# Optimization experiments

Hardware: AMD Instinct MI355X
Metric: run time of the kernel (lower is better)

Reference implementation:

```python
import jax, jax.numpy as jnp
import numpy as np

N, E = 100000, 3200000
IN_DIM, PRED_DIM, REL_NUM = 128, 16, 50
H, L = 4, 3          # heads per layer, num_layers
NEG_SLOPE = 0.2      # SALayer attention leaky_relu slope


def setup_inputs() -> dict:
    key = jax.random.key(0)
    ks = jax.random.split(key, 9)
    hid = IN_DIM // 2
    return {
        "inputs": jax.random.normal(ks[0], (N, IN_DIM), jnp.float32),
        "centrality": jax.random.uniform(ks[1], (N,), jnp.float32),
        # per-head scoring MLP: Linear(in,in/2) -> ReLU -> Linear(in/2,1)
        "W1": jax.random.normal(ks[2], (H, hid, IN_DIM), jnp.float32) * 0.05,
        "b1": jnp.zeros((H, hid), jnp.float32),
        "W2": jax.random.normal(ks[3], (H, hid), jnp.float32) * 0.05,
        "b2": jnp.zeros((H,), jnp.float32),
        "rel_emb": jax.random.normal(ks[4], (REL_NUM, PRED_DIM), jnp.float32),
        # per-layer predicate->attention projection (pred_dim -> heads)
        "W_pred": jax.random.normal(ks[5], (L, PRED_DIM, H), jnp.float32) * 0.1,
        "gamma": jnp.ones((1, H), jnp.float32),
        "beta": jnp.zeros((1, H), jnp.float32),
        "edge_types": jax.random.randint(ks[6], (E,), 0, REL_NUM),
        "src": jax.random.randint(ks[7], (E,), 0, N),
        "dst": jax.random.randint(ks[8], (E,), 0, N),
    }


def _edge_softmax(e, dst, n):
    # numerically stable softmax over incoming edges of each dst node, per head
    m = jax.ops.segment_max(e, dst, num_segments=n)          # (N,H)
    ex = jnp.exp(e - m[dst])                                  # (E,H)
    s = jax.ops.segment_sum(ex, dst, num_segments=n)          # (N,H)
    return ex / s[dst]


def reference(inputs, centrality, W1, b1, W2, b2, rel_emb, W_pred,
              gamma, beta, edge_types, src, dst):
    n = inputs.shape[0]
    # multi-head scoring MLPs -> per-node per-head scalar scores (N,H)
    hid = jax.nn.relu(jnp.einsum('ni,khi->nkh', inputs, W1) + b1)  # (N,H,hid)
    h = jnp.einsum('nkh,kh->nk', hid, W2) + b2                     # (N,H)
    ef = rel_emb[edge_types]                                       # (E,P)
    for l in range(L):
        # SALayer: predicate-based attention, edge softmax, aggregate src scores
        e = jax.nn.leaky_relu(ef @ W_pred[l], NEG_SLOPE)           # (E,H)
        a = _edge_softmax(e, dst, n)                               # (E,H)
        h = jax.nn.relu(jax.ops.segment_sum(a * h[src], dst, num_segments=n))
        if l != L - 1:
            # flatten(1).mean(-1,keepdim).repeat(1,H)
            h = jnp.repeat(jnp.mean(h, axis=-1, keepdims=True), H, axis=-1)
    logits = h  # (N,H)
    # centrality scaling: leaky_relu(((c*gamma+beta)*logits).mean(-1,keepdim))
    scaled = (centrality[:, None] * gamma + beta) * logits
    return jax.nn.leaky_relu(jnp.mean(scaled, axis=-1, keepdims=True), 0.01)
```

## Files before the change

### kernel.cpp

```cpp
#include <hip/hip_runtime.h>
#include <cstdint>
#include <cstddef>

#define NHEAD 4
#define HID 64
#define NCOL 256
#define INDIM 128
#define PREDDIM 16
#define RELNUM 50
#define NLAYER 3
#define ECHUNK 8192
#define DSHIFT 9
#define DPB 512
#define MAXBUCK 256
#define MAXCHUNK 512
#define SPLIT_BLOCKS 32
#define MLP_GRID 512

typedef _Float16 half8 __attribute__((ext_vector_type(8)));
typedef float float4v __attribute__((ext_vector_type(4)));
typedef const __attribute__((address_space(1))) void gvoid_t;
typedef __attribute__((address_space(3))) void lvoid_t;

__global__ __launch_bounds__(256, 2) void mlp_mfma_kernel(
    const float* __restrict__ X, const _Float16* __restrict__ Wh,
    const _Float16* __restrict__ Wl, const float* __restrict__ b1,
    const float* __restrict__ W2, const float* __restrict__ b2,
    float* __restrict__ h0, int N)
{
    __shared__ float Xs[2][64][128];

    const int tid  = threadIdx.x;
    const int w    = tid >> 6;
    const int lane = tid & 63;
    const int n16  = lane & 15;
    const int q    = lane >> 4;
    const int swzm = (n16 & 7) << 4;

    half8 bh[4][4], bl[4][4];
    float b1v[4], w2v[4];
    #pragma unroll
    for (int ct = 0; ct < 4; ct++) {
        const int c = w * 64 + ct * 16 + n16;
        const _Float16* pb = Wh + (size_t)c * INDIM + q * 8;
        const _Float16* pl = Wl + (size_t)c * INDIM + q * 8;
        #pragma unroll
        for (int ks = 0; ks < 4; ks++) {
            bh[ct][ks] = *reinterpret_cast<const half8*>(pb + ks * 32);
            bl[ct][ks] = *reinterpret_cast<const half8*>(pl + ks * 32);
        }
        b1v[ct] = b1[c];
        w2v[ct] = W2[c];
    }
    #pragma unroll
    for (int ct = 0; ct < 4; ct++) {
        #pragma unroll
        for (int ks = 0; ks < 4; ks++)
            asm volatile("" : "+v"(bh[ct][ks]), "+v"(bl[ct][ks]));
        asm volatile("" : "+v"(b1v[ct]), "+v"(w2v[ct]));
    }

    const float bk = b2[w];
    const int ntiles = (N + 63) >> 6;

    auto stage = [&](int tile, int buf) {
        #pragma unroll
        for (int i = 0; i < 8; i++) {
            const int lds_off = i * 4096 + w * 1024 + lane * 16;
            const int node = lds_off >> 9;
            const int scol = (lds_off & 511) ^ ((node & 7) << 4);
            const int gn = min(tile * 64 + node, N - 1);
            const char* gsrc = (const char*)X + (size_t)gn * 512 + scol;
            char* ldst = (char*)(&Xs[buf][0][0]) + lds_off;
            __builtin_amdgcn_global_load_lds((gvoid_t*)gsrc, (lvoid_t*)ldst,
                                             16, 0, 0);
        }
    };

    int tile = blockIdx.x;
    if (tile >= ntiles) return;
    int buf = 0;
    stage(tile, 0);
    asm volatile("s_waitcnt vmcnt(0)" ::: "memory");
    __syncthreads();

    while (true) {
        const int nxt = tile + MLP_GRID;
        if (nxt < ntiles) stage(nxt, buf ^ 1);

        #pragma unroll 1
        for (int mt = 0; mt < 4; mt++) {
            const char* rowp = (const char*)(&Xs[buf][mt * 16 + n16][0]);
            half8 ah[4], al[4];
            #pragma unroll
            for (int ks = 0; ks < 4; ks++) {
                const int cb0 = ks * 128 + q * 32;
                float4v r0 = *reinterpret_cast<const float4v*>(rowp + (cb0 ^ swzm));
                float4v r1 = *reinterpret_cast<const float4v*>(rowp + ((cb0 + 16) ^ swzm));
                #pragma unroll
                for (int j = 0; j < 4; j++) {
                    float x = r0[j];
                    _Float16 hh = (_Float16)x;
                    ah[ks][j] = hh;
                    al[ks][j] = (_Float16)((x - (float)hh) * 2048.0f);
                    x = r1[j];
                    hh = (_Float16)x;
                    ah[ks][4 + j] = hh;
                    al[ks][4 + j] = (_Float16)((x - (float)hh) * 2048.0f);
                }
            }

            float s[4] = {0.f, 0.f, 0.f, 0.f};
            #pragma unroll
            for (int ct = 0; ct < 4; ct++) {
                float4v acc = (float4v){0.f,0.f,0.f,0.f};
                float4v aca = (float4v){0.f,0.f,0.f,0.f};
                float4v acb = (float4v){0.f,0.f,0.f,0.f};
                #pragma unroll
                for (int ks = 0; ks < 4; ks++) {
                    acc = __builtin_amdgcn_mfma_f32_16x16x32_f16(ah[ks], bh[ct][ks], acc, 0, 0, 0);
                    aca = __builtin_amdgcn_mfma_f32_16x16x32_f16(ah[ks], bl[ct][ks], aca, 0, 0, 0);
                    acb = __builtin_amdgcn_mfma_f32_16x16x32_f16(al[ks], bh[ct][ks], acb, 0, 0, 0);
                }
                #pragma unroll
                for (int r = 0; r < 4; r++) {
                    float v = acc[r] + (aca[r] + acb[r]) * (1.0f / 2048.0f) + b1v[ct];
                    s[r] += fmaxf(v, 0.f) * w2v[ct];
                }
            }

            #pragma unroll
            for (int r = 0; r < 4; r++) {
                float v = s[r];
                v += __shfl_down(v, 8, 16);
                v += __shfl_down(v, 4, 16);
                v += __shfl_down(v, 2, 16);
                v += __shfl_down(v, 1, 16);
                if (n16 == 0) {
                    int node = tile * 64 + mt * 16 + q * 4 + r;
                    if (node < N) h0[(size_t)node * NHEAD + w] = v + bk;
                }
            }
        }

        if (nxt >= ntiles) break;
        asm volatile("s_waitcnt vmcnt(0)" ::: "memory");
        __syncthreads();
        tile = nxt;
        buf ^= 1;
    }
}

__global__ __launch_bounds__(1024) void bucket_count_fused_kernel(
    const int* __restrict__ dst, int* __restrict__ blockhist, int E,
    int nbuck, int nb,
    const float* __restrict__ rel_emb, const float* __restrict__ W_pred,
    float* __restrict__ wtab,
    const float* __restrict__ W1, _Float16* __restrict__ Wh,
    _Float16* __restrict__ Wl)
{
    __shared__ int hist[MAXBUCK];
    const int tid = threadIdx.x;
    const int bx  = blockIdx.x;

    if (bx < nb) {
        if (tid < MAXBUCK) hist[tid] = 0;
        __syncthreads();
        const int base = bx * ECHUNK;
        const int end  = min(base + ECHUNK, E);
        const int nvec = (end - base) >> 2;
        const int4* d4p = reinterpret_cast<const int4*>(dst + base);
        for (int g = tid; g < nvec; g += 1024) {
            int4 d = d4p[g];
            atomicAdd(&hist[d.x >> DSHIFT], 1);
            atomicAdd(&hist[d.y >> DSHIFT], 1);
            atomicAdd(&hist[d.z >> DSHIFT], 1);
            atomicAdd(&hist[d.w >> DSHIFT], 1);
        }
        for (int i = base + (nvec << 2) + tid; i < end; i += 1024)
            atomicAdd(&hist[dst[i] >> DSHIFT], 1);
        __syncthreads();
        if (tid < nbuck) blockhist[(size_t)tid * nb + bx] = hist[tid];
    } else if (bx == nb) {
        const int idx = tid;
        if (idx < NLAYER * RELNUM * NHEAD) {
            int h = idx & 3;
            int qq = idx >> 2;
            int t = qq % RELNUM;
            int l = qq / RELNUM;
            float acc = 0.f;
            #pragma unroll
            for (int p = 0; p < PREDDIM; p++)
                acc = fmaf(rel_emb[t * PREDDIM + p],
                           W_pred[l * PREDDIM * NHEAD + p * NHEAD + h], acc);
            float e = (acc >= 0.f) ? acc : 0.2f * acc;
            wtab[idx] = __expf(e);
        }
    } else {
        const int i = (bx - nb - 1) * 1024 + tid;
        float v = W1[i];
        _Float16 h = (_Float16)v;
        Wh[i] = h;
        Wl[i] = (_Float16)((v - (float)h) * 2048.0f);
    }
}

__global__ __launch_bounds__(512) void scan_chunks_kernel(
    const int* __restrict__ blockhist, int* __restrict__ blockbase,
    int* __restrict__ bucket_size, int nb)
{
    __shared__ int s[MAXCHUNK];
    const int b = blockIdx.x;
    const int t = threadIdx.x;
    int v = (t < nb) ? blockhist[(size_t)b * nb + t] : 0;
    s[t] = v;
    __syncthreads();
    for (int off = 1; off < MAXCHUNK; off <<= 1) {
        int u = (t >= off) ? s[t - off] : 0;
        __syncthreads();
        s[t] += u;
        __syncthreads();
    }
    if (t < nb) blockbase[(size_t)b * nb + t] = s[t] - v;
    if (t == MAXCHUNK - 1) bucket_size[b] = s[t];
}

__global__ __launch_bounds__(256) void scan_buckets_kernel(
    const int* __restrict__ bucket_size, int* __restrict__ bucket_start, int nbuck)
{
    __shared__ int s[256];
    const int t = threadIdx.x;
    int v = (t < nbuck) ? bucket_size[t] : 0;
    s[t] = v;
    __syncthreads();
    for (int off = 1; off < 256; off <<= 1) {
        int u = (t >= off) ? s[t - off] : 0;
        __syncthreads();
        s[t] += u;
        __syncthreads();
    }
    if (t < nbuck) bucket_start[t] = s[t] - v;
}

__global__ __launch_bounds__(1024) void bucket_scatter_kernel(
    const int* __restrict__ src, const int* __restrict__ dst,
    const int* __restrict__ types, const int* __restrict__ blockbase,
    const int* __restrict__ bucket_start, int* __restrict__ bucketed,
    int E, int nbuck, int nb)
{
    __shared__ int lbase[MAXBUCK];
    __shared__ int cur[MAXBUCK];
    const int tid = threadIdx.x;
    if (tid < MAXBUCK) {
        lbase[tid] = (tid < nbuck)
            ? blockbase[(size_t)tid * nb + blockIdx.x] + bucket_start[tid] : 0;
        cur[tid] = 0;
    }
    __syncthreads();
    const int base = blockIdx.x * ECHUNK;
    const int end  = min(base + ECHUNK, E);
    const int nvec = (end - base) >> 2;
    const int4* s4p = reinterpret_cast<const int4*>(src + base);
    const int4* d4p = reinterpret_cast<const int4*>(dst + base);
    const int4* t4p = reinterpret_cast<const int4*>(types + base);
    for (int g = tid; g < nvec; g += 1024) {
        int4 sv = s4p[g], dv = d4p[g], tv = t4p[g];
        int b, r;
        b = dv.x >> DSHIFT; r = atomicAdd(&cur[b], 1);
        bucketed[lbase[b] + r] = sv.x | (tv.x << 17) | ((dv.x & (DPB - 1)) << 23);
        b = dv.y >> DSHIFT; r = atomicAdd(&cur[b], 1);
        bucketed[lbase[b] + r] = sv.y | (tv.y << 17) | ((dv.y & (DPB - 1)) << 23);
        b = dv.z >> DSHIFT; r = atomicAdd(&cur[b], 1);
        bucketed[lbase[b] + r] = sv.z | (tv.z << 17) | ((dv.z & (DPB - 1)) << 23);
        b = dv.w >> DSHIFT; r = atomicAdd(&cur[b], 1);
        bucketed[lbase[b] + r] = sv.w | (tv.w << 17) | ((dv.w & (DPB - 1)) << 23);
    }
    for (int i = base + (nvec << 2) + tid; i < end; i += 1024) {
        int d = dst[i];
        int b = d >> DSHIFT;
        int r = atomicAdd(&cur[b], 1);
        bucketed[lbase[b] + r] = src[i] | (types[i] << 17) | ((d & (DPB - 1)) << 23);
    }
}

__global__ __launch_bounds__(1024) void bucket_to_csr_kernel(
    const int* __restrict__ bucket_start, const int* __restrict__ bucket_size,
    const int* __restrict__ bucketed, int* __restrict__ sorted,
    int* __restrict__ row_start, int* __restrict__ deg, int N)
{
    __shared__ int cnt[DPB];
    __shared__ int sc[DPB];
    __shared__ int rs[DPB];
    __shared__ int cur[DPB];
    const int tid = threadIdx.x;
    const int b   = blockIdx.x;
    const int d0  = b << DSHIFT;
    const int nd  = min(DPB, N - d0);
    const int s0  = bucket_start[b];
    const int ne  = bucket_size[b];

    if (tid < DPB) { cnt[tid] = 0; cur[tid] = 0; }
    __syncthreads();
    for (int i = tid; i < ne; i += 1024)
        atomicAdd(&cnt[((unsigned)bucketed[s0 + i] >> 23) & (DPB - 1)], 1);
    __syncthreads();
    int v = 0;
    if (tid < DPB) { v = cnt[tid]; sc[tid] = v; }
    __syncthreads();
    for (int off = 1; off < DPB; off <<= 1) {
        int u = (tid < DPB && tid >= off) ? sc[tid - off] : 0;
        __syncthreads();
        if (tid < DPB) sc[tid] += u;
        __syncthreads();
    }
    if (tid < DPB) {
        int ex = sc[tid] - v;
        rs[tid] = s0 + ex;
        if (tid < nd) {
            row_start[d0 + tid] = s0 + ex;
            deg[d0 + tid] = v;
        }
    }
    __syncthreads();
    for (int i = tid; i < ne; i += 1024) {
        int pk = bucketed[s0 + i];
        int d  = ((unsigned)pk >> 23) & (DPB - 1);
        int r  = atomicAdd(&cur[d], 1);
        sorted[rs[d] + r] = pk & 0x7FFFFF;
    }
}

template <int MODE>
__global__ __launch_bounds__(256) void agg_kernel(
    const int* __restrict__ row_start, const int* __restrict__ deg,
    const int* __restrict__ sorted, const float* __restrict__ wt_l,
    const float* __restrict__ hin, float* __restrict__ hout,
    const float* __restrict__ centrality, const float* __restrict__ gamma,
    const float* __restrict__ beta, int N)
{
    __shared__ float4 wt4[RELNUM];
    for (int i = threadIdx.x; i < RELNUM; i += blockDim.x)
        wt4[i] = reinterpret_cast<const float4*>(wt_l)[i];
    __syncthreads();

    int gid = blockIdx.x * blockDim.x + threadIdx.x;
    int d = gid >> 2, j = gid & 3;
    if (d >= N) return;

    int b = row_start[d], n = deg[d];
    float n0 = 0.f, n1 = 0.f, n2 = 0.f, n3 = 0.f;
    float d0 = 0.f, d1 = 0.f, d2 = 0.f, d3 = 0.f;
    for (int i = j; i < n; i += 4) {
        int pk = sorted[b + i];
        int s = pk & 0x1FFFF;
        int t = pk >> 17;
        float4 w4 = wt4[t];
        if (MODE == 0) {
            float4 h4 = *reinterpret_cast<const float4*>(hin + (size_t)s * NHEAD);
            n0 = fmaf(w4.x, h4.x, n0); n1 = fmaf(w4.y, h4.y, n1);
            n2 = fmaf(w4.z, h4.z, n2); n3 = fmaf(w4.w, h4.w, n3);
        } else {
            float hv = hin[s];
            n0 = fmaf(w4.x, hv, n0); n1 = fmaf(w4.y, hv, n1);
            n2 = fmaf(w4.z, hv, n2); n3 = fmaf(w4.w, hv, n3);
        }
        d0 += w4.x; d1 += w4.y; d2 += w4.z; d3 += w4.w;
    }

    #pragma unroll
    for (int k = 1; k <= 2; k <<= 1) {
        n0 += __shfl_xor(n0, k); n1 += __shfl_xor(n1, k);
        n2 += __shfl_xor(n2, k); n3 += __shfl_xor(n3, k);
        d0 += __shfl_xor(d0, k); d1 += __shfl_xor(d1, k);
        d2 += __shfl_xor(d2, k); d3 += __shfl_xor(d3, k);
    }

    if (j == 0) {
        float r0 = (n > 0) ? fmaxf(n0 / d0, 0.f) : 0.f;
        float r1 = (n > 0) ? fmaxf(n1 / d1, 0.f) : 0.f;
        float r2 = (n > 0) ? fmaxf(n2 / d2, 0.f) : 0.f;
        float r3 = (n > 0) ? fmaxf(n3 / d3, 0.f) : 0.f;
        if (MODE == 2) {
            float c = centrality[d];
            r0 *= (c * gamma[0] + beta[0]);
            r1 *= (c * gamma[1] + beta[1]);
            r2 *= (c * gamma[2] + beta[2]);
            r3 *= (c * gamma[3] + beta[3]);
        }
        float m = (r0 + r1 + r2 + r3) * 0.25f;
        if (MODE < 2) hout[d] = m;
        else          hout[d] = (m > 0.f) ? m : 0.01f * m;
    }
}

extern "C" void kernel_launch(void* const* d_in, const int* in_sizes, int n_in,
                              void* d_out, int out_size, void* d_ws, size_t ws_size,
                              hipStream_t stream)
{
    const float* X          = (const float*)d_in[0];
    const float* centrality = (const float*)d_in[1];
    const float* W1         = (const float*)d_in[2];
    const float* b1         = (const float*)d_in[3];
    const float* W2         = (const float*)d_in[4];
    const float* b2         = (const float*)d_in[5];
    const float* rel_emb    = (const float*)d_in[6];
    const float* W_pred     = (const float*)d_in[7];
    const float* gamma      = (const float*)d_in[8];
    const float* beta       = (const float*)d_in[9];
    const int*   edge_types = (const int*)d_in[10];
    const int*   src        = (const int*)d_in[11];
    const int*   dst        = (const int*)d_in[12];
    float* out = (float*)d_out;

    const int N = in_sizes[1];
    const int E = in_sizes[10];
    const int nbuck = (N + DPB - 1) / DPB;
    const int eb = (E + ECHUNK - 1) / ECHUNK;

    char* ws = (char*)d_ws;
    size_t off = 0;
    auto alloc = [&](size_t bytes) -> void* {
        void* p = ws + off;
        off = (off + bytes + 255) & ~(size_t)255;
        return p;
    };
    int*   deg       = (int*)alloc((size_t)N * 4);
    int*   row_start = (int*)alloc((size_t)N * 4);
    int*   bsize     = (int*)alloc((size_t)MAXBUCK * 4);
    int*   bstart    = (int*)alloc((size_t)MAXBUCK * 4);
    int*   blockhist = (int*)alloc((size_t)nbuck * eb * 4);
    int*   blockbase = (int*)alloc((size_t)nbuck * eb * 4);
    int*   bucketed  = (int*)alloc((size_t)E * 4);
    int*   sorted    = (int*)alloc((size_t)E * 4);
    float* wtab      = (float*)alloc((size_t)NLAYER * RELNUM * NHEAD * 4);
    float* h0        = (float*)alloc((size_t)N * NHEAD * 4);
    float* hs        = (float*)alloc((size_t)N * 4);
    float* hs2       = (float*)alloc((size_t)N * 4);
    _Float16* Wh     = (_Float16*)alloc((size_t)NCOL * INDIM * 2);
    _Float16* Wl     = (_Float16*)alloc((size_t)NCOL * INDIM * 2);
    (void)ws_size; (void)n_in; (void)out_size;

    bucket_count_fused_kernel<<<eb + 1 + SPLIT_BLOCKS, 1024, 0, stream>>>(
        dst, blockhist, E, nbuck, eb, rel_emb, W_pred, wtab, W1, Wh, Wl);
    scan_chunks_kernel<<<nbuck, MAXCHUNK, 0, stream>>>(blockhist, blockbase, bsize, eb);
    scan_buckets_kernel<<<1, 256, 0, stream>>>(bsize, bstart, nbuck);
    bucket_scatter_kernel<<<eb, 1024, 0, stream>>>(src, dst, edge_types, blockbase,
                                                   bstart, bucketed, E, nbuck, eb);
    bucket_to_csr_kernel<<<nbuck, 1024, 0, stream>>>(bstart, bsize, bucketed, sorted,
                                                     row_start, deg, N);

    mlp_mfma_kernel<<<MLP_GRID, 256, 0, stream>>>(X, Wh, Wl, b1, W2, b2, h0, N);

    const int ab = (N * NHEAD + 255) / 256;
    agg_kernel<0><<<ab, 256, 0, stream>>>(row_start, deg, sorted, wtab + 0 * RELNUM * NHEAD,
                                          h0, hs, nullptr, nullptr, nullptr, N);
    agg_kernel<1><<<ab, 256, 0, stream>>>(row_start, deg, sorted, wtab + 1 * RELNUM * NHEAD,
                                          hs, hs2, nullptr, nullptr, nullptr, N);
    agg_kernel<2><<<ab, 256, 0, stream>>>(row_start, deg, sorted, wtab + 2 * RELNUM * NHEAD,
                                          hs2, out, centrality, gamma, beta, N);
}
```

Before: 273.1 us.

## Convert MLP inputs to split-fp16 once at staging into MFMA-ready LDS layout

Replaces async global-to-LDS fp32 staging with register prefetch of the next tile. Each thread converts its slice to hi/lo fp16 once and writes it to LDS in an MFMA operand layout. Previously every wave redid the fp32-to-fp16 split on each read. Now the MFMA loop reads half8 operands directly with an XOR swizzle. The cost is 32 more registers per thread for the prefetch, which may pressure occupancy at 2 blocks/SM, and the load-to-LDS overlap now depends on register prefetch.

Result: slower. 283.3 us (+3.7%).

```diff
diff --git a/kernel.cpp b/kernel.cpp
--- a/kernel.cpp
+++ b/kernel.cpp
@@ -19,8 +19,6 @@
 
 typedef _Float16 half8 __attribute__((ext_vector_type(8)));
 typedef float float4v __attribute__((ext_vector_type(4)));
-typedef const __attribute__((address_space(1))) void gvoid_t;
-typedef __attribute__((address_space(3))) void lvoid_t;
 
 __global__ __launch_bounds__(256, 2) void mlp_mfma_kernel(
     const float* __restrict__ X, const _Float16* __restrict__ Wh,
@@ -28,14 +26,14 @@
     const float* __restrict__ W2, const float* __restrict__ b2,
     float* __restrict__ h0, int N)
 {
-    __shared__ float Xs[2][64][128];
+    __shared__ _Float16 hA[2][4][4][64][8];
+    __shared__ _Float16 lA[2][4][4][64][8];
 
     const int tid  = threadIdx.x;
     const int w    = tid >> 6;
     const int lane = tid & 63;
     const int n16  = lane & 15;
     const int q    = lane >> 4;
-    const int swzm = (n16 & 7) << 4;
 
     half8 bh[4][4], bl[4][4];
     float b1v[4], w2v[4];
@@ -63,51 +61,56 @@
     const float bk = b2[w];
     const int ntiles = (N + 63) >> 6;
 
-    auto stage = [&](int tile, int buf) {
-        #pragma unroll
-        for (int i = 0; i < 8; i++) {
-            const int lds_off = i * 4096 + w * 1024 + lane * 16;
-            const int node = lds_off >> 9;
-            const int scol = (lds_off & 511) ^ ((node & 7) << 4);
-            const int gn = min(tile * 64 + node, N - 1);
-            const char* gsrc = (const char*)X + (size_t)gn * 512 + scol;
-            char* ldst = (char*)(&Xs[buf][0][0]) + lds_off;
-            __builtin_amdgcn_global_load_lds((gvoid_t*)gsrc, (lvoid_t*)ldst,
-                                             16, 0, 0);
-        }
-    };
+    const int mg  = tid >> 2, sks = tid & 3;
+    const int smt = mg >> 4,  sm  = mg & 15;
 
     int tile = blockIdx.x;
     if (tile >= ntiles) return;
+
+    {
+        const int gn = min(tile * 64 + mg, N - 1);
+        const float4* Xp = reinterpret_cast<const float4*>(X + (size_t)gn * INDIM + sks * 32);
+        float4 xr[8];
+        #pragma unroll
+        for (int i = 0; i < 8; i++) xr[i] = Xp[i];
+        #pragma unroll
+        for (int qq = 0; qq < 4; qq++) {
+            float xs[8] = { xr[qq*2].x, xr[qq*2].y, xr[qq*2].z, xr[qq*2].w,
+                            xr[qq*2+1].x, xr[qq*2+1].y, xr[qq*2+1].z, xr[qq*2+1].w };
+            half8 hv, lv;
+            #pragma unroll
+            for (int j = 0; j < 8; j++) {
+                _Float16 hh = (_Float16)xs[j];
+                hv[j] = hh;
+                lv[j] = (_Float16)((xs[j] - (float)hh) * 2048.0f);
+            }
+            const int slot = (qq * 16 + sm) ^ (2 * sks);
+            *reinterpret_cast<half8*>(&hA[0][smt][sks][slot][0]) = hv;
+            *reinterpret_cast<half8*>(&lA[0][smt][sks][slot][0]) = lv;
+        }
+    }
+    __syncthreads();
     int buf = 0;
-    stage(tile, 0);
-    asm volatile("s_waitcnt vmcnt(0)" ::: "memory");
-    __syncthreads();
 
     while (true) {
         const int nxt = tile + MLP_GRID;
-        if (nxt < ntiles) stage(nxt, buf ^ 1);
+
+        float4 xn[8];
+        if (nxt < ntiles) {
+            const int gn = min(nxt * 64 + mg, N - 1);
+            const float4* Xp = reinterpret_cast<const float4*>(X + (size_t)gn * INDIM + sks * 32);
+            #pragma unroll
+            for (int i = 0; i < 8; i++) xn[i] = Xp[i];
+        }
 
         #pragma unroll 1
         for (int mt = 0; mt < 4; mt++) {
-            const char* rowp = (const char*)(&Xs[buf][mt * 16 + n16][0]);
             half8 ah[4], al[4];
             #pragma unroll
-            for (int ks = 0; ks < 4; ks++) {
-                const int cb0 = ks * 128 + q * 32;
-                float4v r0 = *reinterpret_cast<const float4v*>(rowp + (cb0 ^ swzm));
-                float4v r1 = *reinterpret_cast<const float4v*>(rowp + ((cb0 + 16) ^ swzm));
-                #pragma unroll
-                for (int j = 0; j < 4; j++) {
-                    float x = r0[j];
-                    _Float16 hh = (_Float16)x;
-                    ah[ks][j] = hh;
-                    al[ks][j] = (_Float16)((x - (float)hh) * 2048.0f);
-                    x = r1[j];
-                    hh = (_Float16)x;
-                    ah[ks][4 + j] = hh;
-                    al[ks][4 + j] = (_Float16)((x - (float)hh) * 2048.0f);
-                }
+            for (int kk = 0; kk < 4; kk++) {
+                const int slot = lane ^ (2 * kk);
+                ah[kk] = *reinterpret_cast<const half8*>(&hA[buf][mt][kk][slot][0]);
+                al[kk] = *reinterpret_cast<const half8*>(&lA[buf][mt][kk][slot][0]);
             }
 
             float s[4] = {0.f, 0.f, 0.f, 0.f};
@@ -117,10 +120,10 @@
                 float4v aca = (float4v){0.f,0.f,0.f,0.f};
                 float4v acb = (float4v){0.f,0.f,0.f,0.f};
                 #pragma unroll
-                for (int ks = 0; ks < 4; ks++) {
-                    acc = __builtin_amdgcn_mfma_f32_16x16x32_f16(ah[ks], bh[ct][ks], acc, 0, 0, 0);
-                    aca = __builtin_amdgcn_mfma_f32_16x16x32_f16(ah[ks], bl[ct][ks], aca, 0, 0, 0);
-                    acb = __builtin_amdgcn_mfma_f32_16x16x32_f16(al[ks], bh[ct][ks], acb, 0, 0, 0);
+                for (int kk = 0; kk < 4; kk++) {
+                    acc = __builtin_amdgcn_mfma_f32_16x16x32_f16(ah[kk], bh[ct][kk], acc, 0, 0, 0);
+                    aca = __builtin_amdgcn_mfma_f32_16x16x32_f16(ah[kk], bl[ct][kk], aca, 0, 0, 0);
+                    acb = __builtin_amdgcn_mfma_f32_16x16x32_f16(al[kk], bh[ct][kk], acb, 0, 0, 0);
                 }
                 #pragma unroll
                 for (int r = 0; r < 4; r++) {
@@ -144,7 +147,22 @@
         }
 
         if (nxt >= ntiles) break;
-        asm volatile("s_waitcnt vmcnt(0)" ::: "memory");
+
+        #pragma unroll
+        for (int qq = 0; qq < 4; qq++) {
+            float xs[8] = { xn[qq*2].x, xn[qq*2].y, xn[qq*2].z, xn[qq*2].w,
+                            xn[qq*2+1].x, xn[qq*2+1].y, xn[qq*2+1].z, xn[qq*2+1].w };
+            half8 hv, lv;
+            #pragma unroll
+            for (int j = 0; j < 8; j++) {
+                _Float16 hh = (_Float16)xs[j];
+                hv[j] = hh;
+                lv[j] = (_Float16)((xs[j] - (float)hh) * 2048.0f);
+            }
+            const int slot = (qq * 16 + sm) ^ (2 * sks);
+            *reinterpret_cast<half8*>(&hA[buf ^ 1][smt][sks][slot][0]) = hv;
+            *reinterpret_cast<half8*>(&lA[buf ^ 1][smt][sks][slot][0]) = lv;
+        }
         __syncthreads();
         tile = nxt;
         buf ^= 1;
```

## Convert MLP input tile to split fp16 once per tile in shared memory

Applied to the files above, without the earlier changes.

Before, each of the four waves converted the same fp32 X tile into hi/lo fp16 fragments, so every wave repeated the whole conversion. Now the block converts the tile once into swizzled fp16 hi/lo LDS buffers, and each wave loads ready-made MFMA fragments. To make room, the fp32 staging buffer is no longer double-buffered, and an extra barrier plus a convert phase sit between the prefetch wait and the compute. This cuts redundant VALU conversion work but shrinks the overlap between the global load and compute.

New measurement: 274.5 us (median of 3 runs). About the same (+0.5%).

```diff
diff --git a/kernel.cpp b/kernel.cpp
--- a/kernel.cpp
+++ b/kernel.cpp
@@ -28,14 +28,15 @@
     const float* __restrict__ W2, const float* __restrict__ b2,
     float* __restrict__ h0, int N)
 {
-    __shared__ float Xs[2][64][128];
+    __shared__ float    Xf[64][128];
+    __shared__ _Float16 hA[4][4][64][8];
+    __shared__ _Float16 lA[4][4][64][8];
 
     const int tid  = threadIdx.x;
     const int w    = tid >> 6;
     const int lane = tid & 63;
     const int n16  = lane & 15;
     const int q    = lane >> 4;
-    const int swzm = (n16 & 7) << 4;
 
     half8 bh[4][4], bl[4][4];
     float b1v[4], w2v[4];
@@ -63,51 +64,70 @@
     const float bk = b2[w];
     const int ntiles = (N + 63) >> 6;
 
-    auto stage = [&](int tile, int buf) {
+    auto stage = [&](int tile) {
         #pragma unroll
         for (int i = 0; i < 8; i++) {
             const int lds_off = i * 4096 + w * 1024 + lane * 16;
-            const int node = lds_off >> 9;
-            const int scol = (lds_off & 511) ^ ((node & 7) << 4);
-            const int gn = min(tile * 64 + node, N - 1);
+            const int row  = lds_off >> 9;
+            const int scol = (lds_off & 511) ^ ((row & 7) << 4);
+            const int gn = min(tile * 64 + row, N - 1);
             const char* gsrc = (const char*)X + (size_t)gn * 512 + scol;
-            char* ldst = (char*)(&Xs[buf][0][0]) + lds_off;
+            char* ldst = (char*)(&Xf[0][0]) + lds_off;
             __builtin_amdgcn_global_load_lds((gvoid_t*)gsrc, (lvoid_t*)ldst,
                                              16, 0, 0);
         }
     };
 
+    const int mg  = tid >> 2, sks = tid & 3;
+    const int smt = mg >> 4,  sm  = mg & 15;
+    const char* frow = (const char*)(&Xf[mg][0]);
+    const int rswz = (mg & 7) << 4;
+
+    auto convert = [&]() {
+        #pragma unroll
+        for (int qq = 0; qq < 4; qq++) {
+            const int cb = sks * 128 + qq * 32;
+            float4v r0 = *reinterpret_cast<const float4v*>(frow + (cb ^ rswz));
+            float4v r1 = *reinterpret_cast<const float4v*>(frow + ((cb + 16) ^ rswz));
+            half8 hv, lv;
+            #pragma unroll
+            for (int j = 0; j < 4; j++) {
+                float x = r0[j];
+                _Float16 hh = (_Float16)x;
+                hv[j] = hh;
+                lv[j] = (_Float16)((x - (float)hh) * 2048.0f);
+                x = r1[j];
+                hh = (_Float16)x;
+                hv[4 + j] = hh;
+                lv[4 + j] = (_Float16)((x - (float)hh) * 2048.0f);
+            }
+            const int slot = (qq * 16 + sm) ^ (2 * sks);
+            *reinterpret_cast<half8*>(&hA[smt][sks][slot][0]) = hv;
+            *reinterpret_cast<half8*>(&lA[smt][sks][slot][0]) = lv;
+        }
+    };
+
     int tile = blockIdx.x;
     if (tile >= ntiles) return;
-    int buf = 0;
-    stage(tile, 0);
+
+    stage(tile);
     asm volatile("s_waitcnt vmcnt(0)" ::: "memory");
+    __syncthreads();
+    convert();
     __syncthreads();
 
     while (true) {
         const int nxt = tile + MLP_GRID;
-        if (nxt < ntiles) stage(nxt, buf ^ 1);
+        if (nxt < ntiles) stage(nxt);
 
         #pragma unroll 1
         for (int mt = 0; mt < 4; mt++) {
-            const char* rowp = (const char*)(&Xs[buf][mt * 16 + n16][0]);
             half8 ah[4], al[4];
             #pragma unroll
-            for (int ks = 0; ks < 4; ks++) {
-                const int cb0 = ks * 128 + q * 32;
-                float4v r0 = *reinterpret_cast<const float4v*>(rowp + (cb0 ^ swzm));
-                float4v r1 = *reinterpret_cast<const float4v*>(rowp + ((cb0 + 16) ^ swzm));
-                #pragma unroll
-                for (int j = 0; j < 4; j++) {
-                    float x = r0[j];
-                    _Float16 hh = (_Float16)x;
-                    ah[ks][j] = hh;
-                    al[ks][j] = (_Float16)((x - (float)hh) * 2048.0f);
-                    x = r1[j];
-                    hh = (_Float16)x;
-                    ah[ks][4 + j] = hh;
-                    al[ks][4 + j] = (_Float16)((x - (float)hh) * 2048.0f);
-                }
+            for (int kk = 0; kk < 4; kk++) {
+                const int slot = lane ^ (2 * kk);
+                ah[kk] = *reinterpret_cast<const half8*>(&hA[mt][kk][slot][0]);
+                al[kk] = *reinterpret_cast<const half8*>(&lA[mt][kk][slot][0]);
             }
 
             float s[4] = {0.f, 0.f, 0.f, 0.f};
@@ -117,10 +137,10 @@
                 float4v aca = (float4v){0.f,0.f,0.f,0.f};
                 float4v acb = (float4v){0.f,0.f,0.f,0.f};
                 #pragma unroll
-                for (int ks = 0; ks < 4; ks++) {
-                    acc = __builtin_amdgcn_mfma_f32_16x16x32_f16(ah[ks], bh[ct][ks], acc, 0, 0, 0);
-                    aca = __builtin_amdgcn_mfma_f32_16x16x32_f16(ah[ks], bl[ct][ks], aca, 0, 0, 0);
-                    acb = __builtin_amdgcn_mfma_f32_16x16x32_f16(al[ks], bh[ct][ks], acb, 0, 0, 0);
+                for (int kk = 0; kk < 4; kk++) {
+                    acc = __builtin_amdgcn_mfma_f32_16x16x32_f16(ah[kk], bh[ct][kk], acc, 0, 0, 0);
+                    aca = __builtin_amdgcn_mfma_f32_16x16x32_f16(ah[kk], bl[ct][kk], aca, 0, 0, 0);
+                    acb = __builtin_amdgcn_mfma_f32_16x16x32_f16(al[kk], bh[ct][kk], acb, 0, 0, 0);
                 }
                 #pragma unroll
                 for (int r = 0; r < 4; r++) {
@@ -144,10 +164,12 @@
         }
 
         if (nxt >= ntiles) break;
+
         asm volatile("s_waitcnt vmcnt(0)" ::: "memory");
         __syncthreads();
+        convert();
+        __syncthreads();
         tile = nxt;
-        buf ^= 1;
     }
 }
 
```
